# Optimization experiments

Hardware: AMD Instinct MI355X
Metric: run time of the kernel (lower is better)

## Reference

```python
import jax, jax.numpy as jnp
import numpy as np

NOPE = 128          # qk_nope_head_dim
ROPE = 64           # qk_rope_head_dim
KV_LORA = 512       # kv_lora_rank
SCALE = (KV_LORA + ROPE) ** (-0.5)


def setup_inputs() -> dict:
    key = jax.random.key(0)
    k1, k2, k3, k4, k5 = jax.random.split(key, 5)
    T, H, K, S = 512, 128, 512, 8192
    q = jax.random.normal(k1, (T, H, NOPE + ROPE), dtype=jnp.float32)
    kv_cache = jax.random.normal(k2, (S, KV_LORA + ROPE), dtype=jnp.float32)
    topk_indices = jax.random.randint(k3, (T, K), 0, S, dtype=jnp.int32)
    k_b_proj_trans = jax.random.normal(k4, (H, KV_LORA, NOPE), dtype=jnp.float32) * 0.02
    v_b_proj = jax.random.normal(k5, (H, 128, KV_LORA), dtype=jnp.float32) * 0.02
    return {"q": q, "kv_cache": kv_cache, "topk_indices": topk_indices,
            "k_b_proj_trans": k_b_proj_trans, "v_b_proj": v_b_proj}


def reference(q, kv_cache, topk_indices, k_b_proj_trans, v_b_proj):
    # q: [T, H, 192]; kv_cache: [S, 576]; topk_indices: [T, K]
    q_nope, q_rope = q[..., :NOPE], q[..., NOPE:]
    # bmm_out(q_nope_t, k_b_proj_trans.transpose(1,2)): [T,H,128] x [H,512,128] -> [T,H,512]
    q_lat = jnp.einsum('thd,hkd->thk', q_nope, k_b_proj_trans)
    q_concat = jnp.concatenate([q_lat, q_rope], axis=-1)        # [T, H, 576]
    # sparse MLA: gather selected latent KV per token
    kv_sel = kv_cache[topk_indices]                              # [T, K, 576]
    scores = jnp.einsum('thc,tkc->thk', q_concat, kv_sel) * SCALE
    p = jax.nn.softmax(scores, axis=-1)                          # [T, H, K]
    attn_lat = jnp.einsum('thk,tkc->thc', p, kv_sel[..., :KV_LORA])  # [T, H, 512]
    # bmm_out(attn_lat_t, v_b_proj.transpose(1,2)): [T,H,512] x [H,512,128] -> [T,H,128]
    out = jnp.einsum('thc,hvc->thv', attn_lat, v_b_proj)
    return out
```

## Files before the change

### kernel.cpp

```cpp
#include <hip/hip_runtime.h>
#include <stdint.h>


#define SCALE 0.041666666666666664f

typedef __bf16 bf16x8 __attribute__((ext_vector_type(8)));
typedef float floatx4 __attribute__((ext_vector_type(4)));

static __device__ __forceinline__ unsigned short f2bf(float f) {
  unsigned int u = __builtin_bit_cast(unsigned int, f);
  u += 0x7FFF + ((u >> 16) & 1);
  return (unsigned short)(u >> 16);
}
static __device__ __forceinline__ float bf2f(unsigned short h) {
  unsigned int u = ((unsigned int)h) << 16;
  return __builtin_bit_cast(float, u);
}
static __device__ __forceinline__ unsigned int pack2(float lo, float hi) {
  return (unsigned int)f2bf(lo) | ((unsigned int)f2bf(hi) << 16);
}
static __device__ __forceinline__ void ldsdma16(const void* g, void* l) {
  __builtin_amdgcn_global_load_lds(
      (const __attribute__((address_space(1))) void*)g,
      (__attribute__((address_space(3))) void*)l, 16, 0, 0);
}
static __device__ __forceinline__ void stage8_f32(const float* __restrict__ src,
                                                  unsigned short* dst) {
  const float4* s4 = reinterpret_cast<const float4*>(src);
  float4 v0 = s4[0], v1 = s4[1];
  uint4 o;
  o.x = pack2(v0.x, v0.y); o.y = pack2(v0.z, v0.w);
  o.z = pack2(v1.x, v1.y); o.w = pack2(v1.z, v1.w);
  *reinterpret_cast<uint4*>(dst) = o;
}

static __device__ __forceinline__ void mfma_4x4_s(const unsigned short* As,
                                                  const unsigned short* Bs,
                                                  int wm, int wn, int l15, int quad,
                                                  int bstride, floatx4 acc[4][4]) {
  bf16x8 af[4], bfr[4];
#pragma unroll
  for (int i = 0; i < 4; ++i)
    af[i] = *reinterpret_cast<const bf16x8*>(&As[(wm + i * 16 + l15) * 32 + quad * 8]);
#pragma unroll
  for (int j = 0; j < 4; ++j)
    bfr[j] = *reinterpret_cast<const bf16x8*>(&Bs[(wn + j * 16 + l15) * bstride + quad * 8]);
#pragma unroll
  for (int i = 0; i < 4; ++i)
#pragma unroll
    for (int j = 0; j < 4; ++j)
      acc[i][j] = __builtin_amdgcn_mfma_f32_16x16x32_bf16(af[i], bfr[j], acc[i][j], 0, 0, 0);
}
static __device__ __forceinline__ void mfma_4x4(const unsigned short* As,
                                                const unsigned short* Bs,
                                                int wm, int wn, int l15, int quad,
                                                floatx4 acc[4][4]) {
  mfma_4x4_s(As, Bs, wm, wn, l15, quad, 32, acc);
}

__global__ void kv_convert(const float* __restrict__ kv, unsigned short* __restrict__ kvb) {
  int i = blockIdx.x * 256 + threadIdx.x;
  float4 v = reinterpret_cast<const float4*>(kv)[i];
  ushort4 o;
  o.x = f2bf(v.x); o.y = f2bf(v.y); o.z = f2bf(v.z); o.w = f2bf(v.w);
  reinterpret_cast<ushort4*>(kvb)[i] = o;
}

__global__ void rope_copy(const float* __restrict__ q, unsigned short* __restrict__ qc) {
  int i = blockIdx.x * 256 + threadIdx.x;
  int r = i & 63;
  int th = i >> 6;
  qc[(size_t)th * 576 + 512 + r] = f2bf(q[(size_t)th * 192 + 128 + r] * SCALE);
}

__global__ __launch_bounds__(256) void qlat_gemm(const float* __restrict__ q,
                                                 const float* __restrict__ kb,
                                                 unsigned short* __restrict__ qc) {
  const int h = blockIdx.x;
  const int tm = (blockIdx.y & 3) * 128;
  const int tn = (blockIdx.y >> 2) * 128;
  __shared__ __align__(16) unsigned short As[128 * 32];
  __shared__ __align__(16) unsigned short Bs[128 * 32];
  const int tid = threadIdx.x;
  const int lane = tid & 63, wave = tid >> 6;
  const int wm = (wave & 1) * 64, wn = (wave >> 1) * 64;
  const int l15 = lane & 15, quad = lane >> 4;
  const int r0 = tid >> 2, cg = tid & 3;
  const float* a0 = q + ((size_t)(tm + r0) * 128 + h) * 192 + cg * 8;
  const float* a1 = q + ((size_t)(tm + r0 + 64) * 128 + h) * 192 + cg * 8;
  const float* b0 = kb + ((size_t)h * 512 + tn + r0) * 128 + cg * 8;
  const float* b1 = b0 + (size_t)64 * 128;
  floatx4 acc[4][4] = {};
  for (int ks = 0; ks < 4; ++ks) {
    stage8_f32(a0 + ks * 32, &As[tid * 8]);
    stage8_f32(a1 + ks * 32, &As[2048 + tid * 8]);
    stage8_f32(b0 + ks * 32, &Bs[tid * 8]);
    stage8_f32(b1 + ks * 32, &Bs[2048 + tid * 8]);
    __syncthreads();
    mfma_4x4(As, Bs, wm, wn, l15, quad, acc);
    __syncthreads();
  }
#pragma unroll
  for (int i = 0; i < 4; ++i) {
    const int row = wm + i * 16 + quad * 4;
#pragma unroll
    for (int j = 0; j < 4; ++j) {
      const int col = wn + j * 16 + l15;
#pragma unroll
      for (int r = 0; r < 4; ++r) {
        const int t = tm + row + r;
        qc[((size_t)t * 128 + h) * 576 + tn + col] = f2bf(acc[i][j][r] * SCALE);
      }
    }
  }
}

__global__ __launch_bounds__(256) void scores_gemm(const unsigned short* __restrict__ qc,
                                                   const unsigned short* __restrict__ kvb,
                                                   const int* __restrict__ topk,
                                                   unsigned short* __restrict__ P) {
  const int t = blockIdx.x;
  const int tn = blockIdx.y * 128;
  __shared__ __align__(16) unsigned short As[128 * 32];
  __shared__ __align__(16) unsigned short Bs[128 * 32];
  const int tid = threadIdx.x;
  const int lane = tid & 63, wave = tid >> 6;
  const int wm = (wave & 1) * 64, wn = (wave >> 1) * 64;
  const int l15 = lane & 15, quad = lane >> 4;
  const int r0 = tid >> 2, cg = tid & 3;
  const unsigned short* a0 = qc + ((size_t)t * 128 + r0) * 576 + cg * 8;
  const unsigned short* a1 = a0 + (size_t)64 * 576;
  const int idx0 = topk[t * 512 + tn + r0];
  const int idx1 = topk[t * 512 + tn + r0 + 64];
  const unsigned short* b0 = kvb + (size_t)idx0 * 576 + cg * 8;
  const unsigned short* b1 = kvb + (size_t)idx1 * 576 + cg * 8;
  floatx4 acc[4][4] = {};
  for (int ks = 0; ks < 18; ++ks) {
    ldsdma16(a0 + ks * 32, &As[tid * 8]);
    ldsdma16(a1 + ks * 32, &As[2048 + tid * 8]);
    ldsdma16(b0 + ks * 32, &Bs[tid * 8]);
    ldsdma16(b1 + ks * 32, &Bs[2048 + tid * 8]);
    __syncthreads();
    mfma_4x4(As, Bs, wm, wn, l15, quad, acc);
    __syncthreads();
  }
#pragma unroll
  for (int i = 0; i < 4; ++i) {
    const int row = wm + i * 16 + quad * 4;
#pragma unroll
    for (int j = 0; j < 4; ++j) {
      const int col = tn + wn + j * 16 + l15;
#pragma unroll
      for (int r = 0; r < 4; ++r)
        P[((size_t)t * 128 + row + r) * 512 + col] = f2bf(acc[i][j][r]);
    }
  }
}

__global__ __launch_bounds__(256) void softmax_rows(unsigned short* __restrict__ P) {
  const int row = blockIdx.x * 4 + (threadIdx.x >> 6);
  const int lane = threadIdx.x & 63;
  unsigned short* rp = P + (size_t)row * 512 + lane * 8;
  uint4 raw = *reinterpret_cast<const uint4*>(rp);
  unsigned int w[4] = {raw.x, raw.y, raw.z, raw.w};
  float f[8];
  float mx = -1e30f;
#pragma unroll
  for (int i = 0; i < 8; ++i) {
    f[i] = bf2f((unsigned short)((w[i >> 1] >> ((i & 1) * 16)) & 0xFFFF));
    mx = fmaxf(mx, f[i]);
  }
#pragma unroll
  for (int off = 32; off; off >>= 1) mx = fmaxf(mx, __shfl_xor(mx, off, 64));
  float s = 0.f;
#pragma unroll
  for (int i = 0; i < 8; ++i) { f[i] = __expf(f[i] - mx); s += f[i]; }
#pragma unroll
  for (int off = 32; off; off >>= 1) s += __shfl_xor(s, off, 64);
  const float inv = 1.0f / s;
  uint4 o;
  o.x = pack2(f[0] * inv, f[1] * inv);
  o.y = pack2(f[2] * inv, f[3] * inv);
  o.z = pack2(f[4] * inv, f[5] * inv);
  o.w = pack2(f[6] * inv, f[7] * inv);
  *reinterpret_cast<uint4*>(rp) = o;
}

#define BSTRIDE 40
#define STSTRIDE 132
__global__ __launch_bounds__(256) void attn_gemm(const unsigned short* __restrict__ P,
                                                 const unsigned short* __restrict__ kvb,
                                                 const int* __restrict__ topk,
                                                 unsigned short* __restrict__ alat) {
  const int t = blockIdx.x;
  const int tn = blockIdx.y * 128;
  __shared__ __align__(16) unsigned short As[128 * 32];
  __shared__ __align__(16) unsigned short St[32 * STSTRIDE];
  __shared__ __align__(16) unsigned short Bs[128 * BSTRIDE];
  const int tid = threadIdx.x;
  const int lane = tid & 63, wave = tid >> 6;
  const int wm = (wave & 1) * 64, wn = (wave >> 1) * 64;
  const int l15 = lane & 15, quad = lane >> 4;
  const unsigned short* a0 = P + ((size_t)t * 128 + (tid >> 2)) * 512 + (tid & 3) * 8;
  const unsigned short* a1 = a0 + (size_t)64 * 512;
  const int key0 = tid >> 4;
  const int cs = tid & 15;
  const int kgT = tid & 3;
  const int cp = tid >> 2;
  const int* tkrow = topk + t * 512;
  floatx4 acc[4][4] = {};
  for (int ks = 0; ks < 16; ++ks) {
    ldsdma16(a0 + ks * 32, &As[tid * 8]);
    ldsdma16(a1 + ks * 32, &As[2048 + tid * 8]);
    const int i0 = tkrow[ks * 32 + key0];
    const int i1 = tkrow[ks * 32 + key0 + 16];
    uint4 v0 = *reinterpret_cast<const uint4*>(kvb + (size_t)i0 * 576 + tn + cs * 8);
    uint4 v1 = *reinterpret_cast<const uint4*>(kvb + (size_t)i1 * 576 + tn + cs * 8);
    *reinterpret_cast<uint4*>(&St[key0 * STSTRIDE + cs * 8]) = v0;
    *reinterpret_cast<uint4*>(&St[(key0 + 16) * STSTRIDE + cs * 8]) = v1;
    __syncthreads();
    unsigned int w[8];
#pragma unroll
    for (int i = 0; i < 8; ++i)
      w[i] = *reinterpret_cast<const unsigned int*>(&St[(kgT * 8 + i) * STSTRIDE + cp * 2]);
    unsigned short r0[8], r1[8];
#pragma unroll
    for (int i = 0; i < 8; ++i) {
      r0[i] = (unsigned short)(w[i] & 0xFFFF);
      r1[i] = (unsigned short)(w[i] >> 16);
    }
    *reinterpret_cast<uint4*>(&Bs[(2 * cp) * BSTRIDE + kgT * 8]) =
        *reinterpret_cast<const uint4*>(r0);
    *reinterpret_cast<uint4*>(&Bs[(2 * cp + 1) * BSTRIDE + kgT * 8]) =
        *reinterpret_cast<const uint4*>(r1);
    __syncthreads();
    mfma_4x4_s(As, Bs, wm, wn, l15, quad, BSTRIDE, acc);
    __syncthreads();
  }
#pragma unroll
  for (int i = 0; i < 4; ++i) {
    const int row = wm + i * 16 + quad * 4;
#pragma unroll
    for (int j = 0; j < 4; ++j) {
      const int col = tn + wn + j * 16 + l15;
#pragma unroll
      for (int r = 0; r < 4; ++r)
        alat[((size_t)(row + r) * 512 + t) * 512 + col] = f2bf(acc[i][j][r]);
    }
  }
}

__global__ __launch_bounds__(256) void out_gemm(const unsigned short* __restrict__ alat,
                                                const float* __restrict__ vb,
                                                float* __restrict__ out) {
  const int h = blockIdx.x;
  const int tm = blockIdx.y * 128;
  __shared__ __align__(16) unsigned short As[128 * 32];
  __shared__ __align__(16) unsigned short Bs[128 * 32];
  const int tid = threadIdx.x;
  const int lane = tid & 63, wave = tid >> 6;
  const int wm = (wave & 1) * 64, wn = (wave >> 1) * 64;
  const int l15 = lane & 15, quad = lane >> 4;
  const int r0 = tid >> 2, cg = tid & 3;
  const unsigned short* a0 = alat + ((size_t)h * 512 + tm + r0) * 512 + cg * 8;
  const unsigned short* a1 = a0 + (size_t)64 * 512;
  const float* b0 = vb + ((size_t)h * 128 + r0) * 512 + cg * 8;
  const float* b1 = b0 + (size_t)64 * 512;
  floatx4 acc[4][4] = {};
  for (int ks = 0; ks < 16; ++ks) {
    ldsdma16(a0 + ks * 32, &As[tid * 8]);
    ldsdma16(a1 + ks * 32, &As[2048 + tid * 8]);
    stage8_f32(b0 + ks * 32, &Bs[tid * 8]);
    stage8_f32(b1 + ks * 32, &Bs[2048 + tid * 8]);
    __syncthreads();
    mfma_4x4(As, Bs, wm, wn, l15, quad, acc);
    __syncthreads();
  }
#pragma unroll
  for (int i = 0; i < 4; ++i) {
    const int row = wm + i * 16 + quad * 4;
#pragma unroll
    for (int j = 0; j < 4; ++j) {
      const int col = wn + j * 16 + l15;
#pragma unroll
      for (int r = 0; r < 4; ++r) {
        const int t = tm + row + r;
        out[((size_t)t * 128 + h) * 128 + col] = acc[i][j][r];
      }
    }
  }
}

extern "C" void kernel_launch(void* const* d_in, const int* in_sizes, int n_in,
                              void* d_out, int out_size, void* d_ws, size_t ws_size,
                              hipStream_t stream) {
  const float* q = (const float*)d_in[0];
  const float* kv = (const float*)d_in[1];
  const int* topk = (const int*)d_in[2];
  const float* kb = (const float*)d_in[3];
  const float* vb = (const float*)d_in[4];
  float* out = (float*)d_out;

  char* ws = (char*)d_ws;
  unsigned short* kvb = (unsigned short*)ws;
  unsigned short* qc = (unsigned short*)(ws + 9437184);
  unsigned short* alat = qc;
  unsigned short* P = (unsigned short*)(ws + 9437184 + 75497472);

  kv_convert<<<dim3(4608), dim3(256), 0, stream>>>(kv, kvb);
  rope_copy<<<dim3(16384), dim3(256), 0, stream>>>(q, qc);
  qlat_gemm<<<dim3(128, 16), dim3(256), 0, stream>>>(q, kb, qc);
  scores_gemm<<<dim3(512, 4), dim3(256), 0, stream>>>(qc, kvb, topk, P);
  softmax_rows<<<dim3(16384), dim3(256), 0, stream>>>(P);
  attn_gemm<<<dim3(512, 4), dim3(256), 0, stream>>>(P, kvb, topk, alat);
  out_gemm<<<dim3(128, 4), dim3(256), 0, stream>>>(alat, vb, out);
}
```

Before: 397.5 us.

## Double-buffer attn_gemm KV gathers and read pre-tiled P from registers

softmax_rows now writes probabilities into a separate buffer, laid out in 32-key tiles ordered by head, so attn_gemm can load its A fragments straight from global memory into registers. The gathered KV rows go through async LDS DMA into a double-buffered staging area, and the next step's gather and A loads are issued before the MFMAs of the current step. Buffer roles change: P2 reuses the qc region and alat reuses the P region. This removes one barrier per step and the A-tile LDS staging, in exchange for more registers and uncoalesced-looking per-lane global loads of A.

```diff
diff --git a/kernel.cpp b/kernel.cpp
--- a/kernel.cpp
+++ b/kernel.cpp
@@ -34,28 +34,22 @@
   *reinterpret_cast<uint4*>(dst) = o;
 }
 
-static __device__ __forceinline__ void mfma_4x4_s(const unsigned short* As,
-                                                  const unsigned short* Bs,
-                                                  int wm, int wn, int l15, int quad,
-                                                  int bstride, floatx4 acc[4][4]) {
-  bf16x8 af[4], bfr[4];
-#pragma unroll
-  for (int i = 0; i < 4; ++i)
-    af[i] = *reinterpret_cast<const bf16x8*>(&As[(wm + i * 16 + l15) * 32 + quad * 8]);
-#pragma unroll
-  for (int j = 0; j < 4; ++j)
-    bfr[j] = *reinterpret_cast<const bf16x8*>(&Bs[(wn + j * 16 + l15) * bstride + quad * 8]);
-#pragma unroll
-  for (int i = 0; i < 4; ++i)
-#pragma unroll
-    for (int j = 0; j < 4; ++j)
-      acc[i][j] = __builtin_amdgcn_mfma_f32_16x16x32_bf16(af[i], bfr[j], acc[i][j], 0, 0, 0);
-}
 static __device__ __forceinline__ void mfma_4x4(const unsigned short* As,
                                                 const unsigned short* Bs,
                                                 int wm, int wn, int l15, int quad,
                                                 floatx4 acc[4][4]) {
-  mfma_4x4_s(As, Bs, wm, wn, l15, quad, 32, acc);
+  bf16x8 af[4], bfr[4];
+#pragma unroll
+  for (int i = 0; i < 4; ++i)
+    af[i] = *reinterpret_cast<const bf16x8*>(&As[(wm + i * 16 + l15) * 32 + quad * 8]);
+#pragma unroll
+  for (int j = 0; j < 4; ++j)
+    bfr[j] = *reinterpret_cast<const bf16x8*>(&Bs[(wn + j * 16 + l15) * 32 + quad * 8]);
+#pragma unroll
+  for (int i = 0; i < 4; ++i)
+#pragma unroll
+    for (int j = 0; j < 4; ++j)
+      acc[i][j] = __builtin_amdgcn_mfma_f32_16x16x32_bf16(af[i], bfr[j], acc[i][j], 0, 0, 0);
 }
 
 __global__ void kv_convert(const float* __restrict__ kv, unsigned short* __restrict__ kvb) {
@@ -157,10 +151,12 @@
   }
 }
 
-__global__ __launch_bounds__(256) void softmax_rows(unsigned short* __restrict__ P) {
+__global__ __launch_bounds__(256) void softmax_rows(const unsigned short* __restrict__ Pin,
+                                                    unsigned short* __restrict__ P2) {
   const int row = blockIdx.x * 4 + (threadIdx.x >> 6);
+  const int t = row >> 7, h = row & 127;
   const int lane = threadIdx.x & 63;
-  unsigned short* rp = P + (size_t)row * 512 + lane * 8;
+  const unsigned short* rp = Pin + (size_t)row * 512 + lane * 8;
   uint4 raw = *reinterpret_cast<const uint4*>(rp);
   unsigned int w[4] = {raw.x, raw.y, raw.z, raw.w};
   float f[8];
@@ -183,46 +179,50 @@
   o.y = pack2(f[2] * inv, f[3] * inv);
   o.z = pack2(f[4] * inv, f[5] * inv);
   o.w = pack2(f[6] * inv, f[7] * inv);
-  *reinterpret_cast<uint4*>(rp) = o;
+  unsigned short* wp =
+      P2 + (((size_t)t * 16 + (lane >> 2)) * 128 + h) * 32 + (lane & 3) * 8;
+  *reinterpret_cast<uint4*>(wp) = o;
 }
 
 #define BSTRIDE 40
-#define STSTRIDE 132
-__global__ __launch_bounds__(256) void attn_gemm(const unsigned short* __restrict__ P,
+__global__ __launch_bounds__(256) void attn_gemm(const unsigned short* __restrict__ P2,
                                                  const unsigned short* __restrict__ kvb,
                                                  const int* __restrict__ topk,
                                                  unsigned short* __restrict__ alat) {
   const int t = blockIdx.x;
   const int tn = blockIdx.y * 128;
-  __shared__ __align__(16) unsigned short As[128 * 32];
-  __shared__ __align__(16) unsigned short St[32 * STSTRIDE];
+  __shared__ __align__(16) unsigned short St[2][32 * 128];
   __shared__ __align__(16) unsigned short Bs[128 * BSTRIDE];
   const int tid = threadIdx.x;
   const int lane = tid & 63, wave = tid >> 6;
   const int wm = (wave & 1) * 64, wn = (wave >> 1) * 64;
   const int l15 = lane & 15, quad = lane >> 4;
-  const unsigned short* a0 = P + ((size_t)t * 128 + (tid >> 2)) * 512 + (tid & 3) * 8;
-  const unsigned short* a1 = a0 + (size_t)64 * 512;
   const int key0 = tid >> 4;
   const int cs = tid & 15;
   const int kgT = tid & 3;
   const int cp = tid >> 2;
   const int* tkrow = topk + t * 512;
+  const unsigned short* a_base =
+      P2 + ((size_t)t * 16 * 128 + wm + l15) * 32 + quad * 8;
   floatx4 acc[4][4] = {};
+  bf16x8 a_cur[4], a_nxt[4];
+  {
+    const int i0 = tkrow[key0];
+    const int i1 = tkrow[16 + key0];
+    ldsdma16(kvb + (size_t)i0 * 576 + tn + cs * 8, &St[0][tid * 8]);
+    ldsdma16(kvb + (size_t)i1 * 576 + tn + cs * 8, &St[0][2048 + tid * 8]);
+#pragma unroll
+    for (int i = 0; i < 4; ++i)
+      a_cur[i] = *reinterpret_cast<const bf16x8*>(a_base + (size_t)i * 16 * 32);
+  }
+  __syncthreads();
+  int cur = 0;
   for (int ks = 0; ks < 16; ++ks) {
-    ldsdma16(a0 + ks * 32, &As[tid * 8]);
-    ldsdma16(a1 + ks * 32, &As[2048 + tid * 8]);
-    const int i0 = tkrow[ks * 32 + key0];
-    const int i1 = tkrow[ks * 32 + key0 + 16];
-    uint4 v0 = *reinterpret_cast<const uint4*>(kvb + (size_t)i0 * 576 + tn + cs * 8);
-    uint4 v1 = *reinterpret_cast<const uint4*>(kvb + (size_t)i1 * 576 + tn + cs * 8);
-    *reinterpret_cast<uint4*>(&St[key0 * STSTRIDE + cs * 8]) = v0;
-    *reinterpret_cast<uint4*>(&St[(key0 + 16) * STSTRIDE + cs * 8]) = v1;
-    __syncthreads();
     unsigned int w[8];
 #pragma unroll
     for (int i = 0; i < 8; ++i)
-      w[i] = *reinterpret_cast<const unsigned int*>(&St[(kgT * 8 + i) * STSTRIDE + cp * 2]);
+      w[i] = *reinterpret_cast<const unsigned int*>(
+          &St[cur][(kgT * 8 + i) * 128 + cp * 2]);
     unsigned short r0[8], r1[8];
 #pragma unroll
     for (int i = 0; i < 8; ++i) {
@@ -234,8 +234,31 @@
     *reinterpret_cast<uint4*>(&Bs[(2 * cp + 1) * BSTRIDE + kgT * 8]) =
         *reinterpret_cast<const uint4*>(r1);
     __syncthreads();
-    mfma_4x4_s(As, Bs, wm, wn, l15, quad, BSTRIDE, acc);
-    __syncthreads();
+    if (ks < 15) {
+      const int i0 = tkrow[(ks + 1) * 32 + key0];
+      const int i1 = tkrow[(ks + 1) * 32 + 16 + key0];
+      ldsdma16(kvb + (size_t)i0 * 576 + tn + cs * 8, &St[cur ^ 1][tid * 8]);
+      ldsdma16(kvb + (size_t)i1 * 576 + tn + cs * 8, &St[cur ^ 1][2048 + tid * 8]);
+#pragma unroll
+      for (int i = 0; i < 4; ++i)
+        a_nxt[i] = *reinterpret_cast<const bf16x8*>(
+            a_base + ((size_t)(ks + 1) * 128 + i * 16) * 32);
+    }
+    bf16x8 bfr[4];
+#pragma unroll
+    for (int j = 0; j < 4; ++j)
+      bfr[j] = *reinterpret_cast<const bf16x8*>(
+          &Bs[(wn + j * 16 + l15) * BSTRIDE + quad * 8]);
+#pragma unroll
+    for (int i = 0; i < 4; ++i)
+#pragma unroll
+      for (int j = 0; j < 4; ++j)
+        acc[i][j] =
+            __builtin_amdgcn_mfma_f32_16x16x32_bf16(a_cur[i], bfr[j], acc[i][j], 0, 0, 0);
+    __syncthreads();
+#pragma unroll
+    for (int i = 0; i < 4; ++i) a_cur[i] = a_nxt[i];
+    cur ^= 1;
   }
 #pragma unroll
   for (int i = 0; i < 4; ++i) {
@@ -304,14 +327,15 @@
   char* ws = (char*)d_ws;
   unsigned short* kvb = (unsigned short*)ws;
   unsigned short* qc = (unsigned short*)(ws + 9437184);
-  unsigned short* alat = qc;
   unsigned short* P = (unsigned short*)(ws + 9437184 + 75497472);
+  unsigned short* P2 = qc;
+  unsigned short* alat = P;
 
   kv_convert<<<dim3(4608), dim3(256), 0, stream>>>(kv, kvb);
   rope_copy<<<dim3(16384), dim3(256), 0, stream>>>(q, qc);
   qlat_gemm<<<dim3(128, 16), dim3(256), 0, stream>>>(q, kb, qc);
   scores_gemm<<<dim3(512, 4), dim3(256), 0, stream>>>(qc, kvb, topk, P);
-  softmax_rows<<<dim3(16384), dim3(256), 0, stream>>>(P);
-  attn_gemm<<<dim3(512, 4), dim3(256), 0, stream>>>(P, kvb, topk, alat);
+  softmax_rows<<<dim3(16384), dim3(256), 0, stream>>>(P, P2);
+  attn_gemm<<<dim3(512, 4), dim3(256), 0, stream>>>(P2, kvb, topk, alat);
   out_gemm<<<dim3(128, 4), dim3(256), 0, stream>>>(alat, vb, out);
 }
```

Result: no change. 393.1 us (-1.1%).
